# Performance work log

Measured on AMD Instinct MI355X. Metric: run time of the kernel, lower is better.

Reference implementation:

```python
import jax, jax.numpy as jnp
import numpy as np

N, D, H, E, K, C = 8192, 1024, 2048, 8, 2, 2560  # tokens, d_model, hidden, experts, top_k, capacity


def setup_inputs() -> dict:
    key = jax.random.key(0)
    ks = jax.random.split(key, 8)
    s_in, s_h = 1.0 / np.sqrt(D), 1.0 / np.sqrt(H)
    return {
        "x": jax.random.normal(ks[0], (N, D), jnp.float32),
        "Wg": jax.random.uniform(ks[1], (D, E), jnp.float32, -s_in, s_in),
        "bg": jnp.zeros((E,), jnp.float32),
        "W1": jax.random.uniform(ks[2], (E, D, H), jnp.float32, -s_in, s_in),
        "b1": jnp.zeros((E, H), jnp.float32),
        "W2": jax.random.uniform(ks[3], (E, H, H), jnp.float32, -s_h, s_h),
        "b2": jnp.zeros((E, H), jnp.float32),
    }


def reference(x, Wg, bg, W1, b1, W2, b2):
    n = x.shape[0]
    logits = x @ Wg + bg                                  # [N, E]
    probs = jax.nn.softmax(logits, axis=-1)
    topk_probs, topk_idx = jax.lax.top_k(probs, K)        # [N, K]

    # auxiliary losses (training mode)
    importance = probs.sum(0)
    importance_loss = jnp.var(importance) / (E ** 2)
    rows = jnp.arange(n)[:, None]
    mask = jnp.zeros_like(probs).at[rows, topk_idx].set(1.0)
    routing_probs = probs * mask
    expert_usage = mask.mean(0)
    routing_weights = routing_probs.mean(0)
    load_balance_loss = E * (expert_usage * routing_weights).sum()
    aux_loss = importance_loss + load_balance_loss

    # dispatch: rank of each (token, k) slot within its expert, in flat order
    flat_e = topk_idx.reshape(-1)                          # [N*K]
    flat_p = topk_probs.reshape(-1)                        # [N*K]
    sample_idx = jnp.repeat(jnp.arange(n), K)              # [N*K]
    oh = (flat_e[:, None] == jnp.arange(E)[None, :]).astype(jnp.int32)  # [N*K, E]
    rank = jnp.take_along_axis(jnp.cumsum(oh, axis=0), flat_e[:, None], axis=1)[:, 0] - 1
    keep = rank < C                                        # capacity truncation (first-come)
    r_safe = jnp.where(keep, rank, C)                      # C is out-of-bounds -> dropped

    buf = jnp.zeros((E, C, D), x.dtype).at[flat_e, r_safe].set(x[sample_idx], mode="drop")
    h = jax.nn.gelu(jnp.einsum("ecd,edh->ech", buf, W1) + b1[:, None, :], approximate=False)
    y = jnp.einsum("ech,eho->eco", h, W2) + b2[:, None, :]  # [E, C, H]

    gathered = y[flat_e, jnp.minimum(r_safe, C - 1)]       # [N*K, H]
    weighted = gathered * (flat_p * keep.astype(x.dtype))[:, None]
    outputs = jnp.zeros((n, H), x.dtype).at[sample_idx].add(weighted)
    return outputs, aux_loss
```

## Files before the change

### kernel.cpp

```cpp
#include <hip/hip_runtime.h>
#include <math.h>
#include <stdint.h>

#define N_TOK 8192
#define DMODEL 1024
#define HID 2048
#define NEXP 8
#define TOPK 2
#define CAP 2560

typedef __bf16 bf16x8 __attribute__((ext_vector_type(8)));
typedef float f32x4 __attribute__((ext_vector_type(4)));
typedef unsigned int u32x4 __attribute__((ext_vector_type(4)));

__device__ __forceinline__ unsigned short f2b(float f) {
    unsigned int u = __builtin_bit_cast(unsigned int, f);
    u += 0x7fffu + ((u >> 16) & 1u);
    return (unsigned short)(u >> 16);
}
__device__ __forceinline__ float b2f(unsigned short s) {
    unsigned int u = ((unsigned int)s) << 16;
    return __builtin_bit_cast(float, u);
}

__device__ __forceinline__ float gelu_f(float v) {
    const float ax = fabsf(v) * 0.70710678118654752440f;
    const float t = __builtin_amdgcn_rcpf(1.f + 0.3275911f * ax);
    float poly = ((((1.061405429f * t - 1.453152027f) * t + 1.421413741f) * t
                   - 0.284496736f) * t + 0.254829592f) * t;
    float er = 1.f - poly * __expf(-ax * ax);
    er = (v >= 0.f) ? er : -er;
    return 0.5f * v * (1.f + er);
}

__device__ __forceinline__ void gload_lds16(const void* g, void* lds) {
    __builtin_amdgcn_global_load_lds(
        (const __attribute__((address_space(1))) unsigned int*)(uintptr_t)g,
        (__attribute__((address_space(3))) unsigned int*)(unsigned int)(uintptr_t)lds,
        16, 0, 0);
}

__global__ __launch_bounds__(256) void gate_kernel(
    const float* __restrict__ x, const float* __restrict__ Wg,
    const float* __restrict__ bg,
    int* __restrict__ flat_e, float* __restrict__ flat_p,
    float* __restrict__ imp_part, float* __restrict__ sel_part)
{
    __shared__ float s_imp[4][NEXP];
    __shared__ float s_sel[4][NEXP];
    const int wave = threadIdx.x >> 6;
    const int lane = threadIdx.x & 63;
    const int t = blockIdx.x * 4 + wave;

    float acc[NEXP];
#pragma unroll
    for (int e = 0; e < NEXP; ++e) acc[e] = 0.f;
    const float* xr = x + (size_t)t * DMODEL;
    for (int d = lane; d < DMODEL; d += 64) {
        const float xv = xr[d];
#pragma unroll
        for (int e = 0; e < NEXP; ++e) acc[e] += xv * Wg[d * NEXP + e];
    }
#pragma unroll
    for (int off = 32; off > 0; off >>= 1) {
#pragma unroll
        for (int e = 0; e < NEXP; ++e) acc[e] += __shfl_xor(acc[e], off);
    }
    float lg[NEXP], mx = -1e30f;
#pragma unroll
    for (int e = 0; e < NEXP; ++e) { lg[e] = acc[e] + bg[e]; mx = fmaxf(mx, lg[e]); }
    float p[NEXP], s = 0.f;
#pragma unroll
    for (int e = 0; e < NEXP; ++e) { p[e] = expf(lg[e] - mx); s += p[e]; }
    const float inv = 1.f / s;
#pragma unroll
    for (int e = 0; e < NEXP; ++e) p[e] *= inv;

    int i0 = 0;
#pragma unroll
    for (int e = 1; e < NEXP; ++e) if (p[e] > p[i0]) i0 = e;
    int i1 = (i0 == 0) ? 1 : 0;
#pragma unroll
    for (int e = 0; e < NEXP; ++e) if (e != i0 && p[e] > p[i1]) i1 = e;

    if (lane == 0) {
        flat_e[2 * t] = i0;  flat_e[2 * t + 1] = i1;
        flat_p[2 * t] = p[i0]; flat_p[2 * t + 1] = p[i1];
#pragma unroll
        for (int e = 0; e < NEXP; ++e) {
            s_imp[wave][e] = p[e];
            s_sel[wave][e] = (e == i0) ? p[i0] : ((e == i1) ? p[i1] : 0.f);
        }
    }
    __syncthreads();
    if (threadIdx.x < NEXP) {
        const int e = threadIdx.x;
        float a = 0.f, b = 0.f;
#pragma unroll
        for (int w = 0; w < 4; ++w) { a += s_imp[w][e]; b += s_sel[w][e]; }
        imp_part[blockIdx.x * NEXP + e] = a;
        sel_part[blockIdx.x * NEXP + e] = b;
    }
}

__global__ __launch_bounds__(1024) void scan_kernel(
    const int* __restrict__ flat_e, int* __restrict__ slot_rank,
    int* __restrict__ row_token, int* __restrict__ n_kept,
    int* __restrict__ cnt_full)
{
    __shared__ int wave_tot[16][NEXP];
    __shared__ int base[NEXP];
    const int tid = threadIdx.x, lane = tid & 63, w = tid >> 6;
    if (tid < NEXP) base[tid] = 0;
    __syncthreads();
    const unsigned long long ltmask =
        (lane == 0) ? 0ull : (~0ull >> (64 - lane));
    for (int chunk = 0; chunk < (N_TOK * TOPK) / 1024; ++chunk) {
        const int s = chunk * 1024 + tid;
        const int e = flat_e[s];
        int prefix = 0;
#pragma unroll
        for (int ee = 0; ee < NEXP; ++ee) {
            unsigned long long m = __ballot(e == ee);
            if (ee == e) prefix = __popcll(m & ltmask);
            if (lane == 0) wave_tot[w][ee] = __popcll(m);
        }
        __syncthreads();
        int before = base[e];
        for (int ww = 0; ww < w; ++ww) before += wave_tot[ww][e];
        const int rank = before + prefix;
        slot_rank[s] = rank;
        if (rank < CAP) row_token[e * CAP + rank] = s >> 1;
        __syncthreads();
        if (tid < NEXP) {
            int add = 0;
#pragma unroll
            for (int ww = 0; ww < 16; ++ww) add += wave_tot[ww][tid];
            base[tid] += add;
        }
        __syncthreads();
    }
    for (int i = tid; i < NEXP * CAP; i += 1024) {
        const int ee = i / CAP;
        const int r = i - ee * CAP;
        const int ne = base[ee] < CAP ? base[ee] : CAP;
        if (r >= ne) row_token[i] = N_TOK;
    }
    if (tid < NEXP) {
        n_kept[tid] = min(base[tid], CAP);
        cnt_full[tid] = base[tid];
    }
}

__global__ __launch_bounds__(256) void convert_x(
    const float* __restrict__ x, unsigned short* __restrict__ xbf)
{
    const size_t i = ((size_t)blockIdx.x * 256 + threadIdx.x) * 4;
    float4 v = make_float4(0.f, 0.f, 0.f, 0.f);
    if (i < (size_t)N_TOK * DMODEL) v = *(const float4*)(x + i);
    ushort4 o;
    o.x = f2b(v.x); o.y = f2b(v.y); o.z = f2b(v.z); o.w = f2b(v.w);
    *(ushort4*)(xbf + i) = o;
}

__global__ __launch_bounds__(256) void transpose_cvt(
    const float* __restrict__ W, unsigned short* __restrict__ Wt,
    const int R, const int Cdim)
{
    __shared__ unsigned short s[64][66];
    const int e = blockIdx.z;
    const int c0 = blockIdx.x * 64, r0 = blockIdx.y * 64;
    const float* We = W + (size_t)e * R * Cdim;
    unsigned short* Wte = Wt + (size_t)e * R * Cdim;
    const int tid = threadIdx.x;
    const int lr = tid >> 6;
    const int lc = tid & 63;
#pragma unroll
    for (int i = 0; i < 16; ++i)
        s[lr + i * 4][lc] =
            f2b(__builtin_nontemporal_load(&We[(size_t)(r0 + lr + i * 4) * Cdim + c0 + lc]));
    __syncthreads();
#pragma unroll
    for (int pass = 0; pass < 2; ++pass) {
        const int cc = (tid >> 3) + pass * 32;
        const int rq = (tid & 7) * 8;
        unsigned short v[8];
#pragma unroll
        for (int k = 0; k < 8; ++k) v[k] = s[rq + k][cc];
        u32x4 o;
        o[0] = v[0] | ((unsigned)v[1] << 16); o[1] = v[2] | ((unsigned)v[3] << 16);
        o[2] = v[4] | ((unsigned)v[5] << 16); o[3] = v[6] | ((unsigned)v[7] << 16);
        *(u32x4*)&Wte[(size_t)(c0 + cc) * R + r0 + rq] = o;
    }
}

#define VMGATE4() do { asm volatile("s_waitcnt vmcnt(4)" ::: "memory"); \
                       __builtin_amdgcn_sched_barrier(0); } while (0)
#define VMGATE0() do { asm volatile("s_waitcnt vmcnt(0)" ::: "memory"); \
                       __builtin_amdgcn_sched_barrier(0); } while (0)
#define NOGATE() ((void)0)

#define PHASE(mf0, STAGE_STMT, TAIL_STMT) do {                                   \
    bf16x8 a0 = lda(c, (mf0), 0), a1 = lda(c, (mf0), 1);                         \
    bf16x8 a2 = lda(c, (mf0) + 1, 0), a3 = lda(c, (mf0) + 1, 1);                 \
    STAGE_STMT;                                                                  \
    __builtin_amdgcn_s_barrier();                                                \
    asm volatile("s_waitcnt lgkmcnt(0)" ::: "memory");                           \
    __builtin_amdgcn_sched_barrier(0);                                           \
    __builtin_amdgcn_s_setprio(1);                                               \
    _Pragma("unroll")                                                            \
    for (int nf = 0; nf < 4; ++nf) {                                             \
        acc[(mf0)][nf] = __builtin_amdgcn_mfma_f32_16x16x32_bf16(                \
            a0, bfr[nf][0], acc[(mf0)][nf], 0, 0, 0);                            \
        acc[(mf0)][nf] = __builtin_amdgcn_mfma_f32_16x16x32_bf16(                \
            a1, bfr[nf][1], acc[(mf0)][nf], 0, 0, 0);                            \
        acc[(mf0) + 1][nf] = __builtin_amdgcn_mfma_f32_16x16x32_bf16(            \
            a2, bfr[nf][0], acc[(mf0) + 1][nf], 0, 0, 0);                        \
        acc[(mf0) + 1][nf] = __builtin_amdgcn_mfma_f32_16x16x32_bf16(            \
            a3, bfr[nf][1], acc[(mf0) + 1][nf], 0, 0, 0);                        \
    }                                                                            \
    __builtin_amdgcn_s_setprio(0);                                               \
    TAIL_STMT;                                                                   \
    __builtin_amdgcn_s_barrier();                                                \
} while (0)

template <bool GATHER, bool DO_GELU, bool NT_OUT>
__global__ __launch_bounds__(512, 2) void mfma_gemm256(
    const unsigned short* __restrict__ A,
    const unsigned short* __restrict__ Wt,
    const float* __restrict__ bias,
    unsigned short* __restrict__ out,
    const int* __restrict__ row_token, const int* __restrict__ n_kept,
    const int Kdim)
{
    __shared__ unsigned short smem[81920];

    int bid = blockIdx.x;
    const int cpx = gridDim.x >> 3;
    bid = (bid & 7) * cpx + (bid >> 3);
    const int e = bid / 80;
    const int rem = bid - e * 80;
    const int m0 = (rem >> 3) * 256;
    const int n0 = (rem & 7) * 256;

    const int n_e = n_kept[e];
    if (m0 >= n_e) return;

    const int t = threadIdx.x;
    const int w = t >> 6, lane = t & 63;
    const int wm = w >> 2, wn = w & 3;
    const int l15 = lane & 15, lq = lane >> 4;

    long abase[2][2], bbase[2][2];
#pragma unroll
    for (int h = 0; h < 2; ++h) {
#pragma unroll
        for (int cc = 0; cc < 2; ++cc) {
            const int srow = h * 128 + cc * 64 + (t >> 3);
            const int skoff = ((t & 7) * 8) ^ ((srow & 4) << 2);
            long ar;
            if (GATHER) ar = (long)row_token[e * CAP + m0 + srow] * Kdim;
            else        ar = ((long)e * CAP + m0 + srow) * (long)Kdim;
            abase[h][cc] = ar + skoff;
            bbase[h][cc] = ((long)e * HID + n0 + srow) * (long)Kdim + skoff;
        }
    }

    auto stageA = [&](int buf, int h0, int ktile) {
        const long ko = (long)ktile * 64;
        char* base = (char*)smem + buf * 32768 + h0 * 16384 + w * 1024;
        gload_lds16(A + (h0 ? abase[1][0] : abase[0][0]) + ko, base);
        gload_lds16(A + (h0 ? abase[1][1] : abase[0][1]) + ko, base + 8192);
    };
    auto stageB = [&](int buf, int h0, int ktile) {
        const long ko = (long)ktile * 64;
        char* base = (char*)smem + 65536 + buf * 32768 + h0 * 16384 + w * 1024;
        gload_lds16(Wt + (h0 ? bbase[1][0] : bbase[0][0]) + ko, base);
        gload_lds16(Wt + (h0 ? bbase[1][1] : bbase[0][1]) + ko, base + 8192);
    };

    const int sx = (l15 & 4) << 3;
    const int kbx0 = (lq * 16) ^ sx;
    const int kbx1 = (64 + lq * 16) ^ sx;
    auto lda = [&](int cbuf, int mf, int ks) -> bf16x8 {
        return *(const bf16x8*)((const char*)smem + cbuf * 32768 +
                                (wm * 128 + mf * 16 + l15) * 128 + (ks ? kbx1 : kbx0));
    };
    auto ldb = [&](int cbuf, int nf, int ks) -> bf16x8 {
        return *(const bf16x8*)((const char*)smem + 65536 + cbuf * 32768 +
                                (wn * 64 + nf * 16 + l15) * 128 + (ks ? kbx1 : kbx0));
    };

    f32x4 acc[8][4];
#pragma unroll
    for (int m = 0; m < 8; ++m)
#pragma unroll
        for (int n = 0; n < 4; ++n) acc[m][n] = (f32x4)0.f;

    const int NT = Kdim >> 6;

    stageA(0, 0, 0); stageA(0, 1, 0);
    stageB(0, 0, 0); stageB(0, 1, 0);
    stageB(1, 0, 1); stageB(1, 1, 1);
    VMGATE4();
    __builtin_amdgcn_s_barrier();

    int bcur = 0;
    for (int kt = 0; kt < NT; ++kt) {
        const int c = kt & 1, o = c ^ 1;
        const int ktA = kt + 1;
        const int ktB = kt + 2;
        int bst = bcur + 2; if (bst >= 3) bst -= 3;

        bf16x8 bfr[4][2];
#pragma unroll
        for (int nf = 0; nf < 4; ++nf) {
            bfr[nf][0] = ldb(bcur, nf, 0);
            bfr[nf][1] = ldb(bcur, nf, 1);
        }
        PHASE(0, if (ktA < NT) stageA(o, 0, ktA), NOGATE());
        PHASE(2, if (ktA < NT) stageA(o, 1, ktA), NOGATE());
        PHASE(4, if (ktB < NT) stageB(bst, 0, ktB), NOGATE());
        if (ktB < NT) {
            PHASE(6, stageB(bst, 1, ktB), VMGATE4());
        } else {
            PHASE(6, NOGATE(), VMGATE0());
        }
        bcur = (bcur == 2) ? 0 : bcur + 1;
    }

    const float* be = bias + (size_t)e * HID;
    float bv[4];
#pragma unroll
    for (int nf = 0; nf < 4; ++nf)
        bv[nf] = be[n0 + wn * 64 + nf * 16 + l15];
#pragma unroll
    for (int mf = 0; mf < 8; ++mf) {
#pragma unroll
        for (int j = 0; j < 4; ++j) {
            const int row = m0 + wm * 128 + mf * 16 + lq * 4 + j;
            unsigned short* orow =
                out + ((size_t)e * CAP + row) * HID + n0 + wn * 64 + l15;
#pragma unroll
            for (int nf = 0; nf < 4; ++nf) {
                float v = acc[mf][nf][j] + bv[nf];
                if (DO_GELU) v = gelu_f(v);
                if (NT_OUT) __builtin_nontemporal_store(f2b(v), &orow[nf * 16]);
                else        orow[nf * 16] = f2b(v);
            }
        }
    }
}

__global__ __launch_bounds__(256) void combine_kernel(
    const unsigned short* __restrict__ y, const int* __restrict__ flat_e,
    const float* __restrict__ flat_p, const int* __restrict__ slot_rank,
    float* __restrict__ out)
{
    const int t = blockIdx.x;
    const int e0 = flat_e[2 * t], e1 = flat_e[2 * t + 1];
    const int r0 = slot_rank[2 * t], r1 = slot_rank[2 * t + 1];
    const bool k0 = r0 < CAP, k1 = r1 < CAP;
    const float w0 = k0 ? flat_p[2 * t] : 0.f;
    const float w1 = k1 ? flat_p[2 * t + 1] : 0.f;
    const unsigned short* y0 = y + ((size_t)e0 * CAP + (k0 ? r0 : 0)) * HID;
    const unsigned short* y1 = y + ((size_t)e1 * CAP + (k1 ? r1 : 0)) * HID;
    float* orow = out + (size_t)t * HID;
    const int c = threadIdx.x * 8;
    u32x4 av = k0 ? __builtin_nontemporal_load((const u32x4*)(y0 + c)) : (u32x4)0u;
    u32x4 bv = k1 ? __builtin_nontemporal_load((const u32x4*)(y1 + c)) : (u32x4)0u;
    float o[8];
    auto comb2 = [&](unsigned int a, unsigned int b, float* dst) {
        dst[0] = w0 * b2f((unsigned short)(a & 0xffffu)) +
                 w1 * b2f((unsigned short)(b & 0xffffu));
        dst[1] = w0 * b2f((unsigned short)(a >> 16)) +
                 w1 * b2f((unsigned short)(b >> 16));
    };
    comb2(av[0], bv[0], o + 0); comb2(av[1], bv[1], o + 2);
    comb2(av[2], bv[2], o + 4); comb2(av[3], bv[3], o + 6);
    f32x4 o0 = {o[0], o[1], o[2], o[3]};
    f32x4 o1 = {o[4], o[5], o[6], o[7]};
    __builtin_nontemporal_store(o0, (f32x4*)(orow + c));
    __builtin_nontemporal_store(o1, (f32x4*)(orow + c + 4));
}

__global__ __launch_bounds__(64) void aux_kernel(
    const float* __restrict__ imp_part, const float* __restrict__ sel_part,
    const int* __restrict__ cnt_full, float* __restrict__ out_aux,
    const int nparts)
{
    const int lane = threadIdx.x;
    __shared__ float imp_s[NEXP], sel_s[NEXP];
    for (int e = 0; e < NEXP; ++e) {
        float a = 0.f, b = 0.f;
        for (int i = lane; i < nparts; i += 64) {
            a += imp_part[i * NEXP + e];
            b += sel_part[i * NEXP + e];
        }
#pragma unroll
        for (int off = 32; off > 0; off >>= 1) {
            a += __shfl_xor(a, off);
            b += __shfl_xor(b, off);
        }
        if (lane == 0) { imp_s[e] = a; sel_s[e] = b; }
    }
    __syncthreads();
    if (lane == 0) {
        double mean = 0.0;
        for (int e = 0; e < NEXP; ++e) mean += imp_s[e];
        mean /= NEXP;
        double var = 0.0;
        for (int e = 0; e < NEXP; ++e) {
            const double d = (double)imp_s[e] - mean;
            var += d * d;
        }
        var /= NEXP;
        double load = 0.0;
        for (int e = 0; e < NEXP; ++e)
            load += ((double)cnt_full[e] / N_TOK) * ((double)sel_s[e] / N_TOK);
        load *= NEXP;
        out_aux[0] = (float)(var / (NEXP * NEXP) + load);
    }
}

extern "C" void kernel_launch(void* const* d_in, const int* in_sizes, int n_in,
                              void* d_out, int out_size, void* d_ws, size_t ws_size,
                              hipStream_t stream) {
    const float* x  = (const float*)d_in[0];
    const float* Wg = (const float*)d_in[1];
    const float* bg = (const float*)d_in[2];
    const float* W1 = (const float*)d_in[3];
    const float* b1 = (const float*)d_in[4];
    const float* W2 = (const float*)d_in[5];
    const float* b2 = (const float*)d_in[6];
    float* out = (float*)d_out;
    (void)in_sizes; (void)n_in; (void)out_size; (void)ws_size;

    char* ws = (char*)d_ws;
    size_t off = 0;
    auto alloc = [&](size_t bytes) -> void* {
        void* p = ws + off;
        off = (off + bytes + 255) & ~(size_t)255;
        return p;
    };
    int*   n_kept    = (int*)alloc(NEXP * sizeof(int));
    int*   cnt_full  = (int*)alloc(NEXP * sizeof(int));
    int*   flat_e    = (int*)alloc((size_t)N_TOK * TOPK * sizeof(int));
    float* flat_p    = (float*)alloc((size_t)N_TOK * TOPK * sizeof(float));
    int*   slot_rank = (int*)alloc((size_t)N_TOK * TOPK * sizeof(int));
    int*   row_tok   = (int*)alloc((size_t)NEXP * CAP * sizeof(int));
    float* imp_part  = (float*)alloc((size_t)(N_TOK / 4) * NEXP * sizeof(float));
    float* sel_part  = (float*)alloc((size_t)(N_TOK / 4) * NEXP * sizeof(float));
    unsigned short* xbf  = (unsigned short*)alloc((size_t)(N_TOK + 1) * DMODEL * 2);
    unsigned short* w1t  = (unsigned short*)alloc((size_t)NEXP * DMODEL * HID * 2);
    unsigned short* w2t  = (unsigned short*)alloc((size_t)NEXP * HID * HID * 2);
    unsigned short* hbuf = (unsigned short*)alloc((size_t)NEXP * CAP * HID * 2);
    unsigned short* ybuf = (unsigned short*)alloc((size_t)NEXP * CAP * HID * 2);

    convert_x<<<(N_TOK + 1) * DMODEL / 1024, 256, 0, stream>>>(x, xbf);
    gate_kernel<<<N_TOK / 4, 256, 0, stream>>>(x, Wg, bg, flat_e, flat_p,
                                               imp_part, sel_part);
    scan_kernel<<<1, 1024, 0, stream>>>(flat_e, slot_rank, row_tok, n_kept, cnt_full);

    const int nblk = NEXP * (CAP / 256) * (HID / 256);

    transpose_cvt<<<dim3(HID / 64, DMODEL / 64, NEXP), 256, 0, stream>>>(W1, w1t, DMODEL, HID);
    mfma_gemm256<true,  true,  false><<<nblk, 512, 0, stream>>>(
        xbf,  w1t, b1, hbuf, row_tok, n_kept, DMODEL);

    transpose_cvt<<<dim3(HID / 64, HID / 64, NEXP), 256, 0, stream>>>(W2, w2t, HID, HID);
    mfma_gemm256<false, false, true ><<<nblk, 512, 0, stream>>>(
        hbuf, w2t, b2, ybuf, row_tok, n_kept, HID);

    combine_kernel<<<N_TOK, 256, 0, stream>>>(ybuf, flat_e, flat_p, slot_rank, out);
    aux_kernel<<<1, 64, 0, stream>>>(imp_part, sel_part, cnt_full,
                                     out + (size_t)N_TOK * HID, N_TOK / 4);
}
```

Before: 488.1 us.

## Make expert GEMMs persistent with atomic tile queue and fuse x conversion into gate

Converts both expert GEMMs into persistent kernels with 256 workgroups that pull 256x256 tiles from a global atomic counter, iterating m-fastest within each expert and n-tile, and skipping tiles beyond the kept row count. The bf16 conversion of x moves into the gate kernel, which removes one launch and one extra read of x. The scan kernel now resets the tile counters and zeroes the padding row. Non-temporal output stores are dropped and occupancy drops to one workgroup per CU, which costs some latency hiding and adds an atomic round-trip per tile.

```diff
diff --git a/kernel.cpp b/kernel.cpp
--- a/kernel.cpp
+++ b/kernel.cpp
@@ -8,6 +8,7 @@
 #define NEXP 8
 #define TOPK 2
 #define CAP 2560
+#define NTILES 640
 
 typedef __bf16 bf16x8 __attribute__((ext_vector_type(8)));
 typedef float f32x4 __attribute__((ext_vector_type(4)));
@@ -44,7 +45,8 @@
     const float* __restrict__ x, const float* __restrict__ Wg,
     const float* __restrict__ bg,
     int* __restrict__ flat_e, float* __restrict__ flat_p,
-    float* __restrict__ imp_part, float* __restrict__ sel_part)
+    float* __restrict__ imp_part, float* __restrict__ sel_part,
+    unsigned short* __restrict__ xbf)
 {
     __shared__ float s_imp[4][NEXP];
     __shared__ float s_sel[4][NEXP];
@@ -56,8 +58,10 @@
 #pragma unroll
     for (int e = 0; e < NEXP; ++e) acc[e] = 0.f;
     const float* xr = x + (size_t)t * DMODEL;
+    unsigned short* xbr = xbf + (size_t)t * DMODEL;
     for (int d = lane; d < DMODEL; d += 64) {
         const float xv = xr[d];
+        xbr[d] = f2b(xv);
 #pragma unroll
         for (int e = 0; e < NEXP; ++e) acc[e] += xv * Wg[d * NEXP + e];
     }
@@ -106,12 +110,15 @@
 __global__ __launch_bounds__(1024) void scan_kernel(
     const int* __restrict__ flat_e, int* __restrict__ slot_rank,
     int* __restrict__ row_token, int* __restrict__ n_kept,
-    int* __restrict__ cnt_full)
+    int* __restrict__ cnt_full, unsigned short* __restrict__ xbf_pad,
+    int* __restrict__ ctrs)
 {
     __shared__ int wave_tot[16][NEXP];
     __shared__ int base[NEXP];
     const int tid = threadIdx.x, lane = tid & 63, w = tid >> 6;
     if (tid < NEXP) base[tid] = 0;
+    if (tid < 2) ctrs[tid] = 0;
+    for (int i = tid; i < DMODEL; i += 1024) xbf_pad[i] = 0;
     __syncthreads();
     const unsigned long long ltmask =
         (lane == 0) ? 0ull : (~0ull >> (64 - lane));
@@ -150,17 +157,6 @@
         n_kept[tid] = min(base[tid], CAP);
         cnt_full[tid] = base[tid];
     }
-}
-
-__global__ __launch_bounds__(256) void convert_x(
-    const float* __restrict__ x, unsigned short* __restrict__ xbf)
-{
-    const size_t i = ((size_t)blockIdx.x * 256 + threadIdx.x) * 4;
-    float4 v = make_float4(0.f, 0.f, 0.f, 0.f);
-    if (i < (size_t)N_TOK * DMODEL) v = *(const float4*)(x + i);
-    ushort4 o;
-    o.x = f2b(v.x); o.y = f2b(v.y); o.z = f2b(v.z); o.w = f2b(v.w);
-    *(ushort4*)(xbf + i) = o;
 }
 
 __global__ __launch_bounds__(256) void transpose_cvt(
@@ -224,60 +220,24 @@
     __builtin_amdgcn_s_barrier();                                                \
 } while (0)
 
-template <bool GATHER, bool DO_GELU, bool NT_OUT>
-__global__ __launch_bounds__(512, 2) void mfma_gemm256(
+template <bool GATHER, bool DO_GELU>
+__global__ __launch_bounds__(512, 1) void mfma_gemm256(
     const unsigned short* __restrict__ A,
     const unsigned short* __restrict__ Wt,
     const float* __restrict__ bias,
     unsigned short* __restrict__ out,
     const int* __restrict__ row_token, const int* __restrict__ n_kept,
-    const int Kdim)
+    int* __restrict__ ctr, const int Kdim)
 {
     __shared__ unsigned short smem[81920];
-
-    int bid = blockIdx.x;
-    const int cpx = gridDim.x >> 3;
-    bid = (bid & 7) * cpx + (bid >> 3);
-    const int e = bid / 80;
-    const int rem = bid - e * 80;
-    const int m0 = (rem >> 3) * 256;
-    const int n0 = (rem & 7) * 256;
-
-    const int n_e = n_kept[e];
-    if (m0 >= n_e) return;
+    int* s_item = (int*)((char*)smem + 163836);
 
     const int t = threadIdx.x;
     const int w = t >> 6, lane = t & 63;
     const int wm = w >> 2, wn = w & 3;
     const int l15 = lane & 15, lq = lane >> 4;
-
-    long abase[2][2], bbase[2][2];
-#pragma unroll
-    for (int h = 0; h < 2; ++h) {
-#pragma unroll
-        for (int cc = 0; cc < 2; ++cc) {
-            const int srow = h * 128 + cc * 64 + (t >> 3);
-            const int skoff = ((t & 7) * 8) ^ ((srow & 4) << 2);
-            long ar;
-            if (GATHER) ar = (long)row_token[e * CAP + m0 + srow] * Kdim;
-            else        ar = ((long)e * CAP + m0 + srow) * (long)Kdim;
-            abase[h][cc] = ar + skoff;
-            bbase[h][cc] = ((long)e * HID + n0 + srow) * (long)Kdim + skoff;
-        }
-    }
-
-    auto stageA = [&](int buf, int h0, int ktile) {
-        const long ko = (long)ktile * 64;
-        char* base = (char*)smem + buf * 32768 + h0 * 16384 + w * 1024;
-        gload_lds16(A + (h0 ? abase[1][0] : abase[0][0]) + ko, base);
-        gload_lds16(A + (h0 ? abase[1][1] : abase[0][1]) + ko, base + 8192);
-    };
-    auto stageB = [&](int buf, int h0, int ktile) {
-        const long ko = (long)ktile * 64;
-        char* base = (char*)smem + 65536 + buf * 32768 + h0 * 16384 + w * 1024;
-        gload_lds16(Wt + (h0 ? bbase[1][0] : bbase[0][0]) + ko, base);
-        gload_lds16(Wt + (h0 ? bbase[1][1] : bbase[0][1]) + ko, base + 8192);
-    };
+    const int srow_lo = t >> 3;
+    const int NT = Kdim >> 6;
 
     const int sx = (l15 & 4) << 3;
     const int kbx0 = (lq * 16) ^ sx;
@@ -291,62 +251,102 @@
                                 (wn * 64 + nf * 16 + l15) * 128 + (ks ? kbx1 : kbx0));
     };
 
-    f32x4 acc[8][4];
-#pragma unroll
-    for (int m = 0; m < 8; ++m)
-#pragma unroll
-        for (int n = 0; n < 4; ++n) acc[m][n] = (f32x4)0.f;
-
-    const int NT = Kdim >> 6;
-
-    stageA(0, 0, 0); stageA(0, 1, 0);
-    stageB(0, 0, 0); stageB(0, 1, 0);
-    stageB(1, 0, 1); stageB(1, 1, 1);
-    VMGATE4();
-    __builtin_amdgcn_s_barrier();
-
-    int bcur = 0;
-    for (int kt = 0; kt < NT; ++kt) {
-        const int c = kt & 1, o = c ^ 1;
-        const int ktA = kt + 1;
-        const int ktB = kt + 2;
-        int bst = bcur + 2; if (bst >= 3) bst -= 3;
-
-        bf16x8 bfr[4][2];
-#pragma unroll
-        for (int nf = 0; nf < 4; ++nf) {
-            bfr[nf][0] = ldb(bcur, nf, 0);
-            bfr[nf][1] = ldb(bcur, nf, 1);
-        }
-        PHASE(0, if (ktA < NT) stageA(o, 0, ktA), NOGATE());
-        PHASE(2, if (ktA < NT) stageA(o, 1, ktA), NOGATE());
-        PHASE(4, if (ktB < NT) stageB(bst, 0, ktB), NOGATE());
-        if (ktB < NT) {
-            PHASE(6, stageB(bst, 1, ktB), VMGATE4());
-        } else {
-            PHASE(6, NOGATE(), VMGATE0());
-        }
-        bcur = (bcur == 2) ? 0 : bcur + 1;
-    }
-
-    const float* be = bias + (size_t)e * HID;
-    float bv[4];
-#pragma unroll
-    for (int nf = 0; nf < 4; ++nf)
-        bv[nf] = be[n0 + wn * 64 + nf * 16 + l15];
-#pragma unroll
-    for (int mf = 0; mf < 8; ++mf) {
-#pragma unroll
-        for (int j = 0; j < 4; ++j) {
-            const int row = m0 + wm * 128 + mf * 16 + lq * 4 + j;
-            unsigned short* orow =
-                out + ((size_t)e * CAP + row) * HID + n0 + wn * 64 + l15;
+    for (;;) {
+        __syncthreads();
+        if (t == 0) *s_item = atomicAdd(ctr, 1);
+        __syncthreads();
+        const int item = *s_item;
+        if (item >= NTILES) break;
+
+        const int e = item / 80;
+        const int rem = item - e * 80;
+        const int m = rem % 10;
+        const int n = rem / 10;
+        const int m0 = m * 256, n0 = n * 256;
+        const int n_e = n_kept[e];
+        if (m0 >= n_e) continue;
+
+        long abase[2][2], bbase[2][2];
+#pragma unroll
+        for (int h = 0; h < 2; ++h) {
+#pragma unroll
+            for (int cc = 0; cc < 2; ++cc) {
+                const int srow = h * 128 + cc * 64 + srow_lo;
+                const int skoff = ((t & 7) * 8) ^ ((srow & 4) << 2);
+                long ar;
+                if (GATHER) ar = (long)row_token[e * CAP + m0 + srow] * Kdim;
+                else        ar = ((long)e * CAP + m0 + srow) * (long)Kdim;
+                abase[h][cc] = ar + skoff;
+                bbase[h][cc] = ((long)e * HID + n0 + srow) * (long)Kdim + skoff;
+            }
+        }
+        auto stageA = [&](int buf, int h0, int ktile) {
+            const long ko = (long)ktile * 64;
+            char* base = (char*)smem + buf * 32768 + h0 * 16384 + w * 1024;
+            gload_lds16(A + (h0 ? abase[1][0] : abase[0][0]) + ko, base);
+            gload_lds16(A + (h0 ? abase[1][1] : abase[0][1]) + ko, base + 8192);
+        };
+        auto stageB = [&](int buf, int h0, int ktile) {
+            const long ko = (long)ktile * 64;
+            char* base = (char*)smem + 65536 + buf * 32768 + h0 * 16384 + w * 1024;
+            gload_lds16(Wt + (h0 ? bbase[1][0] : bbase[0][0]) + ko, base);
+            gload_lds16(Wt + (h0 ? bbase[1][1] : bbase[0][1]) + ko, base + 8192);
+        };
+
+        f32x4 acc[8][4];
+#pragma unroll
+        for (int mm = 0; mm < 8; ++mm)
+#pragma unroll
+            for (int nn = 0; nn < 4; ++nn) acc[mm][nn] = (f32x4)0.f;
+
+        stageA(0, 0, 0); stageA(0, 1, 0);
+        stageB(0, 0, 0); stageB(0, 1, 0);
+        stageB(1, 0, 1); stageB(1, 1, 1);
+        VMGATE4();
+        __builtin_amdgcn_s_barrier();
+
+        int bcur = 0;
+        for (int kt = 0; kt < NT; ++kt) {
+            const int c = kt & 1, o = c ^ 1;
+            const int ktA = kt + 1;
+            const int ktB = kt + 2;
+            int bst = bcur + 2; if (bst >= 3) bst -= 3;
+
+            bf16x8 bfr[4][2];
 #pragma unroll
             for (int nf = 0; nf < 4; ++nf) {
-                float v = acc[mf][nf][j] + bv[nf];
-                if (DO_GELU) v = gelu_f(v);
-                if (NT_OUT) __builtin_nontemporal_store(f2b(v), &orow[nf * 16]);
-                else        orow[nf * 16] = f2b(v);
+                bfr[nf][0] = ldb(bcur, nf, 0);
+                bfr[nf][1] = ldb(bcur, nf, 1);
+            }
+            PHASE(0, if (ktA < NT) stageA(o, 0, ktA), NOGATE());
+            PHASE(2, if (ktA < NT) stageA(o, 1, ktA), NOGATE());
+            PHASE(4, if (ktB < NT) stageB(bst, 0, ktB), NOGATE());
+            if (ktB < NT) {
+                PHASE(6, stageB(bst, 1, ktB), VMGATE4());
+            } else {
+                PHASE(6, NOGATE(), VMGATE0());
+            }
+            bcur = (bcur == 2) ? 0 : bcur + 1;
+        }
+
+        const float* be = bias + (size_t)e * HID;
+        float bv[4];
+#pragma unroll
+        for (int nf = 0; nf < 4; ++nf)
+            bv[nf] = be[n0 + wn * 64 + nf * 16 + l15];
+#pragma unroll
+        for (int mf = 0; mf < 8; ++mf) {
+#pragma unroll
+            for (int j = 0; j < 4; ++j) {
+                const int row = m0 + wm * 128 + mf * 16 + lq * 4 + j;
+                unsigned short* orow =
+                    out + ((size_t)e * CAP + row) * HID + n0 + wn * 64 + l15;
+#pragma unroll
+                for (int nf = 0; nf < 4; ++nf) {
+                    float v = acc[mf][nf][j] + bv[nf];
+                    if (DO_GELU) v = gelu_f(v);
+                    orow[nf * 16] = f2b(v);
+                }
             }
         }
     }
@@ -445,6 +445,7 @@
     };
     int*   n_kept    = (int*)alloc(NEXP * sizeof(int));
     int*   cnt_full  = (int*)alloc(NEXP * sizeof(int));
+    int*   ctrs     = (int*)alloc(2 * sizeof(int));
     int*   flat_e    = (int*)alloc((size_t)N_TOK * TOPK * sizeof(int));
     float* flat_p    = (float*)alloc((size_t)N_TOK * TOPK * sizeof(float));
     int*   slot_rank = (int*)alloc((size_t)N_TOK * TOPK * sizeof(int));
@@ -457,20 +458,19 @@
     unsigned short* hbuf = (unsigned short*)alloc((size_t)NEXP * CAP * HID * 2);
     unsigned short* ybuf = (unsigned short*)alloc((size_t)NEXP * CAP * HID * 2);
 
-    convert_x<<<(N_TOK + 1) * DMODEL / 1024, 256, 0, stream>>>(x, xbf);
     gate_kernel<<<N_TOK / 4, 256, 0, stream>>>(x, Wg, bg, flat_e, flat_p,
-                                               imp_part, sel_part);
-    scan_kernel<<<1, 1024, 0, stream>>>(flat_e, slot_rank, row_tok, n_kept, cnt_full);
-
-    const int nblk = NEXP * (CAP / 256) * (HID / 256);
+                                               imp_part, sel_part, xbf);
+    scan_kernel<<<1, 1024, 0, stream>>>(flat_e, slot_rank, row_tok, n_kept,
+                                        cnt_full, xbf + (size_t)N_TOK * DMODEL,
+                                        ctrs);
 
     transpose_cvt<<<dim3(HID / 64, DMODEL / 64, NEXP), 256, 0, stream>>>(W1, w1t, DMODEL, HID);
-    mfma_gemm256<true,  true,  false><<<nblk, 512, 0, stream>>>(
-        xbf,  w1t, b1, hbuf, row_tok, n_kept, DMODEL);
+    mfma_gemm256<true,  true ><<<256, 512, 0, stream>>>(
+        xbf,  w1t, b1, hbuf, row_tok, n_kept, ctrs + 0, DMODEL);
 
     transpose_cvt<<<dim3(HID / 64, HID / 64, NEXP), 256, 0, stream>>>(W2, w2t, HID, HID);
-    mfma_gemm256<false, false, true ><<<nblk, 512, 0, stream>>>(
-        hbuf, w2t, b2, ybuf, row_tok, n_kept, HID);
+    mfma_gemm256<false, false><<<256, 512, 0, stream>>>(
+        hbuf, w2t, b2, ybuf, row_tok, n_kept, ctrs + 1, HID);
 
     combine_kernel<<<N_TOK, 256, 0, stream>>>(ybuf, flat_e, flat_p, slot_rank, out);
     aux_kernel<<<1, 64, 0, stream>>>(imp_part, sel_part, cnt_full,
```

New measurement: 479.2 us. No clear change (-1.8%).
